# Kernel optimization log

Hardware: AMD Instinct MI355X
Metric: run time of the kernel (lower is better)

The kernel has to match this reference:

```python
import jax, jax.numpy as jnp
import numpy as np

KNB = 64  # max_num_neighbors in torch_geometric radius query


def fps(p, n):
    # Farthest point sampling, deterministic start at index 0. p: [N,3] -> [n] int32
    N = p.shape[0]
    def step(carry, _):
        d, last = carry
        d = jnp.minimum(d, jnp.sum((p - p[last]) ** 2, -1))
        return (d, jnp.argmax(d).astype(jnp.int32)), last
    _, idx = jax.lax.scan(step, (jnp.full((N,), jnp.inf, p.dtype), jnp.int32(0)), None, length=n)
    return idx


def mlp3(h, w1, b1, w2, b2, w3, b3):
    # torch_geometric-style MLP: Lin+ReLU per layer (batch_norm disabled)
    h = jax.nn.relu(h @ w1 + b1)
    h = jax.nn.relu(h @ w2 + b2)
    return jax.nn.relu(h @ w3 + b3)


def sa_module(x, pos, S, r, params):
    # PointNet++ set abstraction: FPS -> ball query -> per-edge MLP -> max pool.
    # x: [B,N,C], pos: [B,N,3] -> ([B,S,Cout], [B,S,3])
    B, N, _ = pos.shape
    idx = jax.vmap(lambda p: fps(p, S))(pos)                           # [B,S]
    ctr = jnp.take_along_axis(pos, idx[:, :, None], 1)                 # [B,S,3]
    d2 = jnp.sum((ctr[:, :, None, :] - pos[:, None, :, :]) ** 2, -1)   # [B,S,N]
    mask = d2 <= r * r
    # first KNB in-radius points in index order (emulates radius() neighbor cap)
    score = jnp.where(mask, (N - jnp.arange(N, dtype=jnp.int32))[None, None, :], 0)
    vals, nb = jax.lax.top_k(score, KNB)                               # [B,S,KNB]
    valid = vals > 0
    flat = nb.reshape(B, S * KNB)
    xj = jnp.take_along_axis(x, flat[:, :, None], 1).reshape(B, S, KNB, -1)
    pj = jnp.take_along_axis(pos, flat[:, :, None], 1).reshape(B, S, KNB, 3)
    feat = jnp.concatenate([xj, pj - ctr[:, :, None, :]], -1)          # [B,S,KNB,C+3]
    h = mlp3(feat, *params)
    h = jnp.where(valid[..., None], h, -jnp.inf)
    return h.max(axis=2), ctr                                          # max-aggr over ball


def setup_inputs() -> dict:
    key = jax.random.key(0)
    ks = jax.random.split(key, 64)
    inp = {}
    inp["x"] = jax.random.normal(ks[0], (16, 2048, 9), jnp.float32)
    inp["pos"] = jax.random.uniform(ks[1], (16, 2048, 3), dtype=jnp.float32)
    i = 2
    for tag, c0, c1, c2, c3 in [("s1", 12, 64, 64, 128), ("s2", 131, 128, 128, 256),
                                 ("s3", 259, 256, 512, 1024), ("f", 1024, 512, 512, 256)]:
        for j, (ci, co) in enumerate([(c0, c1), (c1, c2), (c2, c3)], 1):
            inp[f"{tag}w{j}"] = jax.random.normal(ks[i], (ci, co), jnp.float32) / np.sqrt(ci); i += 1
            inp[f"{tag}b{j}"] = jnp.zeros((co,), jnp.float32)
    for j, (ci, co) in enumerate([(1024, 512), (512, 256), (256, 256), (256, 128), (128, 128)], 1):
        inp[f"l{j}w"] = jax.random.normal(ks[i], (ci, co), jnp.float32) / np.sqrt(ci); i += 1
        inp[f"l{j}b"] = jnp.zeros((co,), jnp.float32)
    return inp


def reference(x, pos,
              s1w1, s1b1, s1w2, s1b2, s1w3, s1b3,
              s2w1, s2b1, s2w2, s2b2, s2w3, s2b3,
              s3w1, s3b1, s3w2, s3b2, s3w3, s3b3,
              fw1, fb1, fw2, fb2, fw3, fb3,
              l1w, l1b, l2w, l2b, l3w, l3b, l4w, l4b, l5w, l5b):
    KP1 = 4  # K+1 frames per sample; B = n_batch*(K+1)
    x1, p1 = sa_module(x, pos, 1024, 0.2, (s1w1, s1b1, s1w2, s1b2, s1w3, s1b3))
    x2, p2 = sa_module(x1, p1, 256, 0.4, (s2w1, s2b1, s2w2, s2b2, s2w3, s2b3))
    # GlobalSAModule: MLP then global max pool over remaining points
    g = mlp3(jnp.concatenate([x2, p2], -1), s3w1, s3b1, s3w2, s3b2, s3w3, s3b3).max(axis=1)  # [B,1024]
    h = jax.nn.relu(g @ l1w + l1b)
    h = jax.nn.relu(h @ l2w + l2b)
    h = h @ l3w + l3b                       # [B,256]
    h = h.reshape(-1, KP1 * 256)            # [n_batch, 1024]
    h = mlp3(h, fw1, fb1, fw2, fb2, fw3, fb3)  # fusion_type == 0
    h = jax.nn.relu(h @ l4w + l4b)
    return h @ l5w + l5b                    # [n_batch, z_dim=128]
```

## Files before the change

kernel.cpp:

```cpp
#include <hip/hip_runtime.h>
#include <cstddef>

#define DEVINF __builtin_inff()

typedef __attribute__((ext_vector_type(8))) short bf16x8;
typedef __attribute__((ext_vector_type(4))) float f32x4;
typedef __attribute__((ext_vector_type(2))) float f32x2;

__device__ __forceinline__ unsigned short f2bf(float x) {
  unsigned u = __float_as_uint(x);
  return (unsigned short)((u + 0x7fff + ((u >> 16) & 1)) >> 16);
}
__device__ __forceinline__ float bf2f(unsigned short h) {
  return __uint_as_float(((unsigned)h) << 16);
}
__device__ __forceinline__ void split_bf(float x, unsigned short& hi, unsigned short& lo) {
  hi = f2bf(x);
  lo = f2bf(x - bf2f(hi));
}

#define FPS_RED_LEVEL(CTRL)                                                      \
  {                                                                              \
    int th = __builtin_amdgcn_update_dpp((int)hi, (int)hi, CTRL, 0xf, 0xf, false); \
    int tl = __builtin_amdgcn_update_dpp((int)lo, (int)lo, CTRL, 0xf, 0xf, false); \
    bool take = ((unsigned)th > hi) || (((unsigned)th == hi) && ((unsigned)tl > lo)); \
    hi = take ? (unsigned)th : hi;                                               \
    lo = take ? (unsigned)tl : lo;                                               \
  }

template <int PPLH, int NCH>
__device__ __forceinline__ unsigned long long fps_wave_step(
    f32x2* qx, f32x2* qy, f32x2* qz, f32x2* d, float lx, float ly, float lz,
    int lane, int ibase) {
#pragma clang fp contract(off)
  const int CH = PPLH / NCH;
  float bv[NCH];
  int bi[NCH];
#pragma unroll
  for (int c = 0; c < NCH; ++c) { bv[c] = -DEVINF; bi[c] = 0x7fffffff; }
  f32x2 lxv = {lx, lx}, lyv = {ly, ly}, lzv = {lz, lz};
#pragma unroll
  for (int h = 0; h < PPLH; ++h) {
    const int c = h / CH;
    f32x2 dx = qx[h] - lxv, dy = qy[h] - lyv, dz = qz[h] - lzv;
    f32x2 t0 = dx * dx, t1 = dy * dy, t2 = dz * dz;
    f32x2 d2 = (t0 + t1) + t2;
    f32x2 dn;
    dn.x = fminf(d[h].x, d2.x);
    dn.y = fminf(d[h].y, d2.y);
    d[h] = dn;
    int i0 = ibase + (2 * h) * 64 + lane;
    if (dn.x > bv[c]) { bv[c] = dn.x; bi[c] = i0; }
    if (dn.y > bv[c]) { bv[c] = dn.y; bi[c] = i0 + 64; }
  }
  unsigned hi, lo;
  if (NCH == 4) {
    unsigned h0 = __float_as_uint(bv[0]), l0 = ~(unsigned)bi[0];
    unsigned h1 = __float_as_uint(bv[1]), l1 = ~(unsigned)bi[1];
    unsigned h2 = __float_as_uint(bv[2]), l2 = ~(unsigned)bi[2];
    unsigned h3 = __float_as_uint(bv[3]), l3 = ~(unsigned)bi[3];
    bool t01 = (h1 > h0) || ((h1 == h0) && (l1 > l0));
    unsigned ha = t01 ? h1 : h0, la = t01 ? l1 : l0;
    bool t23 = (h3 > h2) || ((h3 == h2) && (l3 > l2));
    unsigned hb = t23 ? h3 : h2, lb = t23 ? l3 : l2;
    bool tab = (hb > ha) || ((hb == ha) && (lb > la));
    hi = tab ? hb : ha;
    lo = tab ? lb : la;
  } else {
    const int c1 = (NCH > 1) ? 1 : 0;
    unsigned h0 = __float_as_uint(bv[0]), l0 = ~(unsigned)bi[0];
    unsigned h1 = __float_as_uint(bv[c1]), l1 = ~(unsigned)bi[c1];
    bool t01 = (h1 > h0) || ((h1 == h0) && (l1 > l0));
    hi = t01 ? h1 : h0;
    lo = t01 ? l1 : l0;
  }
  FPS_RED_LEVEL(0x111)
  FPS_RED_LEVEL(0x112)
  FPS_RED_LEVEL(0x114)
  FPS_RED_LEVEL(0x118)
  FPS_RED_LEVEL(0x142)
  FPS_RED_LEVEL(0x143)
  return (((unsigned long long)hi) << 32) | lo;
}

struct PrepJobs {
  const float* src[9];
  unsigned short* hi[9];
  unsigned short* lo[9];
  int K[9], N[9], rl[9];
  int blk0[10];
};

__global__ __launch_bounds__(256, 1) void fps1_prep_kernel(
    const float* __restrict__ pos, float* __restrict__ p1, PrepJobs jb) {
#pragma clang fp contract(off)
  const int tid = threadIdx.x;
  if (blockIdx.x >= 16) {
    int blk = blockIdx.x - 16;
    int j = 0;
#pragma unroll
    for (int t = 1; t < 9; ++t)
      if (blk >= jb.blk0[t]) j = t;
    int idx = (blk - jb.blk0[j]) * 256 + tid;
    int rl = jb.rl[j], N = jb.N[j], K = jb.K[j];
    if (idx >= N * rl) return;
    int n = idx / rl, k = idx - n * rl;
    float v = (k < K) ? jb.src[j][(size_t)k * N + n] : 0.f;
    unsigned short h, l;
    split_bf(v, h, l);
    jb.hi[j][idx] = h;
    jb.lo[j][idx] = l;
    return;
  }
  const int b = blockIdx.x;
  const int w = tid >> 6, lane = tid & 63;
  __shared__ __align__(16) float4 p4[2048];
  __shared__ __align__(16) float4 carr[1024];
  __shared__ unsigned long long kv[2][4];
  f32x2 qx[4], qy[4], qz[4], d[4];
  const int ibase = w * 512;
#pragma unroll
  for (int h = 0; h < 4; ++h) {
    int i0 = ibase + (2 * h) * 64 + lane, i1 = i0 + 64;
    const float* a = pos + ((size_t)b * 2048 + i0) * 3;
    const float* c = pos + ((size_t)b * 2048 + i1) * 3;
    float x0 = a[0], y0 = a[1], z0 = a[2];
    float x1 = c[0], y1 = c[1], z1 = c[2];
    qx[h].x = x0; qx[h].y = x1;
    qy[h].x = y0; qy[h].y = y1;
    qz[h].x = z0; qz[h].y = z1;
    d[h].x = DEVINF; d[h].y = DEVINF;
    p4[i0] = float4{x0, y0, z0, 0.f};
    p4[i1] = float4{x1, y1, z1, 0.f};
  }
  __syncthreads();
  int last = 0;
  for (int s = 0; s < 1024; ++s) {
    float4 c4 = p4[last];
    if (tid == 0) carr[s] = c4;
    unsigned long long k =
        fps_wave_step<4, 4>(qx, qy, qz, d, c4.x, c4.y, c4.z, lane, ibase);
    if (lane == 63) kv[s & 1][w] = k;
    __syncthreads();
    unsigned long long k0 = kv[s & 1][0], k1 = kv[s & 1][1];
    unsigned long long k2 = kv[s & 1][2], k3 = kv[s & 1][3];
    unsigned long long ka = k0 > k1 ? k0 : k1;
    unsigned long long kb = k2 > k3 ? k2 : k3;
    unsigned long long kk = ka > kb ? ka : kb;
    last = (int)~(unsigned)kk;
  }
  for (int i = tid; i < 1024; i += 256) {
    float4 c = carr[i];
    p1[((size_t)b * 1024 + i) * 3 + 0] = c.x;
    p1[((size_t)b * 1024 + i) * 3 + 1] = c.y;
    p1[((size_t)b * 1024 + i) * 3 + 2] = c.z;
  }
}

template <int KS, int T>
__device__ __forceinline__ void mfma_allm(
    const unsigned short* __restrict__ inHi, const unsigned short* __restrict__ inLo,
    int sIn, const unsigned short* __restrict__ wHi,
    const unsigned short* __restrict__ wLo, int rl, const float* __restrict__ bias,
    int n0, int lane, f32x4 acc[4][T]) {
  const int col = lane & 15, quad = lane >> 4;
#pragma unroll
  for (int t = 0; t < T; ++t) {
    float bv = bias[n0 + t * 16 + col];
#pragma unroll
    for (int mt = 0; mt < 4; ++mt) {
      acc[mt][t].x = bv; acc[mt][t].y = bv; acc[mt][t].z = bv; acc[mt][t].w = bv;
    }
  }
  size_t b0 = (size_t)(n0 + col) * rl + quad * 8;
  bf16x8 bh = *(const bf16x8*)(wHi + b0);
  bf16x8 bl = *(const bf16x8*)(wLo + b0);
#pragma unroll 1
  for (int ks = 0; ks < KS; ++ks) {
    bf16x8 ah[4], al[4];
#pragma unroll
    for (int mt = 0; mt < 4; ++mt) {
      int aoff = (mt * 16 + col) * sIn + ks * 32 + quad * 8;
      ah[mt] = *(const bf16x8*)(inHi + aoff);
      al[mt] = *(const bf16x8*)(inLo + aoff);
    }
#pragma unroll
    for (int t = 0; t < T; ++t) {
      int nks = (t + 1 < T) ? ks : ks + 1;
      int nt = (t + 1 < T) ? t + 1 : 0;
      if (nks > KS - 1) nks = KS - 1;
      size_t nboff = (size_t)(n0 + nt * 16 + col) * rl + nks * 32 + quad * 8;
      bf16x8 nh = *(const bf16x8*)(wHi + nboff);
      bf16x8 nl = *(const bf16x8*)(wLo + nboff);
#pragma unroll
      for (int mt = 0; mt < 4; ++mt) {
        acc[mt][t] = __builtin_amdgcn_mfma_f32_16x16x32_bf16(ah[mt], bh, acc[mt][t], 0, 0, 0);
        acc[mt][t] = __builtin_amdgcn_mfma_f32_16x16x32_bf16(ah[mt], bl, acc[mt][t], 0, 0, 0);
        acc[mt][t] = __builtin_amdgcn_mfma_f32_16x16x32_bf16(al[mt], bh, acc[mt][t], 0, 0, 0);
      }
      bh = nh;
      bl = nl;
    }
  }
}

template <int T>
__device__ __forceinline__ void store_allm(const f32x4 acc[4][T], int n0,
                                           unsigned short* outHi,
                                           unsigned short* outLo, int sOut,
                                           int lane) {
  const int col = lane & 15, quad = lane >> 4;
// ... 40 lines not shown
    const unsigned short* __restrict__ inHi, const unsigned short* __restrict__ inLo,
    int sIn, const unsigned short* __restrict__ wHi,
    const unsigned short* __restrict__ wLo, int rl, const float* __restrict__ bias,
    int n0, int lane, f32x4 acc[T]) {
  const int col = lane & 15, quad = lane >> 4;
#pragma unroll
  for (int t = 0; t < T; ++t) {
    float bv = bias[n0 + t * 16 + col];
    acc[t].x = bv; acc[t].y = bv; acc[t].z = bv; acc[t].w = bv;
  }
  size_t b0 = (size_t)(n0 + col) * rl + quad * 8;
  bf16x8 bh = *(const bf16x8*)(wHi + b0);
  bf16x8 bl = *(const bf16x8*)(wLo + b0);
#pragma unroll 1
  for (int ks = 0; ks < KS; ++ks) {
    int aoff = col * sIn + ks * 32 + quad * 8;
    bf16x8 ah = *(const bf16x8*)(inHi + aoff);
    bf16x8 al = *(const bf16x8*)(inLo + aoff);
#pragma unroll
    for (int t = 0; t < T; ++t) {
      int nks = (t + 1 < T) ? ks : ks + 1;
      int nt = (t + 1 < T) ? t + 1 : 0;
      if (nks > KS - 1) nks = KS - 1;
      size_t nboff = (size_t)(n0 + nt * 16 + col) * rl + nks * 32 + quad * 8;
      bf16x8 nh = *(const bf16x8*)(wHi + nboff);
      bf16x8 nl = *(const bf16x8*)(wLo + nboff);
      acc[t] = __builtin_amdgcn_mfma_f32_16x16x32_bf16(ah, bh, acc[t], 0, 0, 0);
      acc[t] = __builtin_amdgcn_mfma_f32_16x16x32_bf16(ah, bl, acc[t], 0, 0, 0);
      acc[t] = __builtin_amdgcn_mfma_f32_16x16x32_bf16(al, bh, acc[t], 0, 0, 0);
      bh = nh;
      bl = nl;
    }
  }
}

template <int T>
__device__ __forceinline__ void store_1m(const f32x4 acc[T], int n0,
                                         unsigned short* outHi,
                                         unsigned short* outLo, int sOut, int lane) {
  const int col = lane & 15, quad = lane >> 4;
#pragma unroll
  for (int t = 0; t < T; ++t)
#pragma unroll
    for (int r = 0; r < 4; ++r) {
      int p = quad * 4 + r;
      float v = fmaxf(acc[t][r], 0.f);
      unsigned short h, l;
      split_bf(v, h, l);
      outHi[p * sOut + n0 + t * 16 + col] = h;
      outLo[p * sOut + n0 + t * 16 + col] = l;
    }
}

__global__ __launch_bounds__(256, 4) void sa1_kernel(
    const float* __restrict__ x,
    const float* __restrict__ pos,
    const float* __restrict__ ctr,
    float* __restrict__ p2,
    const unsigned short* __restrict__ w1h, const unsigned short* __restrict__ w1l,
    const unsigned short* __restrict__ w2h, const unsigned short* __restrict__ w2l,
    const unsigned short* __restrict__ w3h, const unsigned short* __restrict__ w3l,
    const float* __restrict__ b1, const float* __restrict__ b2,
    const float* __restrict__ b3,
    float* __restrict__ out)
{
  const int N = 2048;
  const float r2 = (float)(0.2 * 0.2);
  const int tid = threadIdx.x;
  const int w = tid >> 6, lane = tid & 63;
  __shared__ __align__(16) unsigned short smem[4 * 4608];
  unsigned short* bufA_hi = smem;
  unsigned short* bufA_lo = smem + 4608;
  unsigned short* bufB_hi = smem + 9216;
  unsigned short* bufB_lo = smem + 13824;
  __shared__ int nb[64];
  __shared__ int tot[4];
  __shared__ unsigned long long kv2[2][4];

  if (blockIdx.x < 16) {
    const int bb = blockIdx.x;
    float4* q4 = (float4*)smem;
    float4* carr = (float4*)(smem + 8192);
    for (int i = tid; i < 1024; i += 256) {
      const float* pr = ctr + ((size_t)bb * 1024 + i) * 3;
      q4[i] = float4{pr[0], pr[1], pr[2], 0.f};
    }
    __syncthreads();
    f32x2 qx[2], qy[2], qz[2], d[2];
    const int ibase = w * 256;
#pragma unroll
    for (int h = 0; h < 2; ++h) {
      int i0 = ibase + (2 * h) * 64 + lane, i1 = i0 + 64;
      float4 a = q4[i0], c = q4[i1];
      qx[h].x = a.x; qx[h].y = c.x;
      qy[h].x = a.y; qy[h].y = c.y;
      qz[h].x = a.z; qz[h].y = c.z;
      d[h].x = DEVINF; d[h].y = DEVINF;
    }
    int last = 0;
    for (int s = 0; s < 256; ++s) {
      float4 c4 = q4[last];
      if (tid == 0) carr[s] = c4;
      unsigned long long k =
          fps_wave_step<2, 2>(qx, qy, qz, d, c4.x, c4.y, c4.z, lane, ibase);
      if (lane == 63) kv2[s & 1][w] = k;
      __syncthreads();
      unsigned long long k0 = kv2[s & 1][0], k1 = kv2[s & 1][1];
      unsigned long long k2 = kv2[s & 1][2], k3 = kv2[s & 1][3];
      unsigned long long ka = k0 > k1 ? k0 : k1;
      unsigned long long kb = k2 > k3 ? k2 : k3;
      unsigned long long kk = ka > kb ? ka : kb;
      last = (int)~(unsigned)kk;
    }
    {
      float4 c = carr[tid];
      if (tid < 256) {
        p2[((size_t)bb * 256 + tid) * 3 + 0] = c.x;
        p2[((size_t)bb * 256 + tid) * 3 + 1] = c.y;
        p2[((size_t)bb * 256 + tid) * 3 + 2] = c.z;
      }
    }
    return;
  }

  const int bs = blockIdx.x - 16;
  const int b = bs >> 10;
  const float cx = ctr[bs * 3 + 0], cy = ctr[bs * 3 + 1], cz = ctr[bs * 3 + 2];
  nb[lane] = 0;
  unsigned long long mloc[8];
  {
#pragma clang fp contract(off)
#pragma unroll
    for (int it = 0; it < 8; ++it) {
      int i = (w * 8 + it) * 64 + lane;
      const float* p = pos + ((size_t)b * N + i) * 3;
      float dx = p[0] - cx, dy = p[1] - cy, dz = p[2] - cz;
      float t0 = dx * dx, t1 = dy * dy, t2 = dz * dz;
      float d2 = (t0 + t1) + t2;
      mloc[it] = __ballot(d2 <= r2);
    }
  }
  {
    int mytot = 0;
#pragma unroll
    for (int it = 0; it < 8; ++it) mytot += (int)__popcll(mloc[it]);
    if (lane == 0) tot[w] = mytot;
  }
  __syncthreads();
  const int t0s = tot[0], t1s = tot[1], t2s = tot[2], t3s = tot[3];
  {
    int cnt = (w > 0 ? t0s : 0) + (w > 1 ? t1s : 0) + (w > 2 ? t2s : 0);
#pragma unroll
    for (int it = 0; it < 8; ++it) {
      unsigned long long m = mloc[it];
      bool inr = (m >> lane) & 1;
      int posn = cnt + (int)__popcll(m & ((1ull << lane) - 1ull));
      if (inr && posn < 64) nb[posn] = (w * 8 + it) * 64 + lane;
      cnt += (int)__popcll(m);
    }
  }
  const int total = t0s + t1s + t2s + t3s;
  const int nvalid = total < 64 ? total : 64;
  __syncthreads();
  {
    int j = nb[lane];
    if (w < 3) {
      const float* xr = x + ((size_t)b * N + j) * 9 + w * 3;
      float f0 = xr[0], f1 = xr[1], f2 = xr[2];
      unsigned short h, l;
      split_bf(f0, h, l); bufA_hi[lane * 72 + w * 3 + 0] = h; bufA_lo[lane * 72 + w * 3 + 0] = l;
      split_bf(f1, h, l); bufA_hi[lane * 72 + w * 3 + 1] = h; bufA_lo[lane * 72 + w * 3 + 1] = l;
      split_bf(f2, h, l); bufA_hi[lane * 72 + w * 3 + 2] = h; bufA_lo[lane * 72 + w * 3 + 2] = l;
    } else {
      const float* pr = pos + ((size_t)b * N + j) * 3;
      float rr[3] = {pr[0] - cx, pr[1] - cy, pr[2] - cz};
#pragma unroll
      for (int c = 0; c < 3; ++c) {
        unsigned short h, l;
        split_bf(rr[c], h, l);
        bufA_hi[lane * 72 + 9 + c] = h;
        bufA_lo[lane * 72 + 9 + c] = l;
      }
#pragma unroll
      for (int k = 12; k < 32; ++k) {
        bufA_hi[lane * 72 + k] = 0;
        bufA_lo[lane * 72 + k] = 0;
      }
    }
  }
  __syncthreads();
  {
    f32x4 acc[4][1];
    mfma_allm<1, 1>(bufA_hi, bufA_lo, 72, w1h, w1l, 40, b1, w * 16, lane, acc);
    store_allm<1>(acc, w * 16, bufB_hi, bufB_lo, 72, lane);
  }
  __syncthreads();
  {
    f32x4 acc[4][1];
    mfma_allm<2, 1>(bufB_hi, bufB_lo, 72, w2h, w2l, 72, b2, w * 16, lane, acc);
    store_allm<1>(acc, w * 16, bufA_hi, bufA_lo, 72, lane);
  }
  __syncthreads();
  {
    f32x4 acc[4][2];
    mfma_allm<2, 2>(bufA_hi, bufA_lo, 72, w3h, w3l, 72, b3, w * 32, lane, acc);
    outpool_allm<2>(acc, w * 32, out + (size_t)bs * 128, nvalid, lane);
  }
}

__global__ __launch_bounds__(256, 2) void sa2_kernel(
    const float* __restrict__ x1,
    const float* __restrict__ pos1,
    const float* __restrict__ ctr,
    const unsigned short* __restrict__ w1h, const unsigned short* __restrict__ w1l,
    const unsigned short* __restrict__ w2h, const unsigned short* __restrict__ w2l,
    const unsigned short* __restrict__ w3h, const unsigned short* __restrict__ w3l,
    const float* __restrict__ b1, const float* __restrict__ b2,
    const float* __restrict__ b3,
    float* __restrict__ out)
{
  const int N = 1024;
  const float r2 = (float)(0.4 * 0.4);
  const int bs = blockIdx.x;
  const int b = bs >> 8;
  const int tid = threadIdx.x;
  const int w = tid >> 6, lane = tid & 63;
  const float cx = ctr[bs * 3 + 0], cy = ctr[bs * 3 + 1], cz = ctr[bs * 3 + 2];
  __shared__ __align__(16) unsigned short bufA_hi[64 * 168], bufA_lo[64 * 168];
  __shared__ __align__(16) unsigned short bufB_hi[64 * 136], bufB_lo[64 * 136];
  __shared__ int nb[64];
  __shared__ int tot[4];
  nb[lane] = 0;
  unsigned long long mloc[4];
  {
#pragma clang fp contract(off)
#pragma unroll
    for (int it = 0; it < 4; ++it) {
      int i = (w * 4 + it) * 64 + lane;
      const float* p = pos1 + ((size_t)b * N + i) * 3;
      float dx = p[0] - cx, dy = p[1] - cy, dz = p[2] - cz;
      float t0 = dx * dx, t1 = dy * dy, t2 = dz * dz;
      float d2 = (t0 + t1) + t2;
      mloc[it] = __ballot(d2 <= r2);
    }
  }
  {
    int mytot = 0;
#pragma unroll
    for (int it = 0; it < 4; ++it) mytot += (int)__popcll(mloc[it]);
    if (lane == 0) tot[w] = mytot;
  }
  __syncthreads();
  const int t0s = tot[0], t1s = tot[1], t2s = tot[2], t3s = tot[3];
  {
    int cnt = (w > 0 ? t0s : 0) + (w > 1 ? t1s : 0) + (w > 2 ? t2s : 0);
#pragma unroll
    for (int it = 0; it < 4; ++it) {
      unsigned long long m = mloc[it];
      bool inr = (m >> lane) & 1;
// ... 207 lines not shown
#pragma unroll 4
    for (int k = 0; k < 1024; ++k) {
      float v = A[k];
      a0 = fmaf(v, fw1[(size_t)k * 512 + tid], a0);
      a1 = fmaf(v, fw1[(size_t)k * 512 + tid + 256], a1);
    }
    Bf[tid] = fmaxf(a0, 0.f);
    Bf[tid + 256] = fmaxf(a1, 0.f);
  }
  __syncthreads();
  {
    float a0 = fb2[tid], a1 = fb2[tid + 256];
#pragma unroll 4
    for (int k = 0; k < 512; ++k) {
      float v = Bf[k];
      a0 = fmaf(v, fw2[(size_t)k * 512 + tid], a0);
      a1 = fmaf(v, fw2[(size_t)k * 512 + tid + 256], a1);
    }
    __syncthreads();
    A[tid] = fmaxf(a0, 0.f);
    A[tid + 256] = fmaxf(a1, 0.f);
  }
  __syncthreads();
  {
    float a = fb3[tid];
#pragma unroll 4
    for (int k = 0; k < 512; ++k) a = fmaf(A[k], fw3[(size_t)k * 256 + tid], a);
    __syncthreads();
    Bf[tid] = fmaxf(a, 0.f);
  }
  __syncthreads();
  {
    if (tid < 128) {
      float a = l4b[tid];
#pragma unroll 4
      for (int k = 0; k < 256; ++k) a = fmaf(Bf[k], l4w[(size_t)k * 128 + tid], a);
      A[tid] = fmaxf(a, 0.f);
    }
  }
  __syncthreads();
  {
    if (tid < 128) {
      float a = l5b[tid];
#pragma unroll 4
      for (int k = 0; k < 128; ++k) a = fmaf(A[k], l5w[(size_t)k * 128 + tid], a);
      out[(size_t)m * 128 + tid] = a;
    }
  }
}

extern "C" void kernel_launch(void* const* d_in, const int* in_sizes, int n_in,
                              void* d_out, int out_size, void* d_ws, size_t ws_size,
                              hipStream_t stream) {
  (void)in_sizes; (void)n_in; (void)out_size; (void)ws_size;
  const float* x    = (const float*)d_in[0];
  const float* pos  = (const float*)d_in[1];
  const float* s1w1 = (const float*)d_in[2];  const float* s1b1 = (const float*)d_in[3];
  const float* s1w2 = (const float*)d_in[4];  const float* s1b2 = (const float*)d_in[5];
  const float* s1w3 = (const float*)d_in[6];  const float* s1b3 = (const float*)d_in[7];
  const float* s2w1 = (const float*)d_in[8];  const float* s2b1 = (const float*)d_in[9];
  const float* s2w2 = (const float*)d_in[10]; const float* s2b2 = (const float*)d_in[11];
  const float* s2w3 = (const float*)d_in[12]; const float* s2b3 = (const float*)d_in[13];
  const float* s3w1 = (const float*)d_in[14]; const float* s3b1 = (const float*)d_in[15];
  const float* s3w2 = (const float*)d_in[16]; const float* s3b2 = (const float*)d_in[17];
  const float* s3w3 = (const float*)d_in[18]; const float* s3b3 = (const float*)d_in[19];
  const float* fw1  = (const float*)d_in[20]; const float* fb1  = (const float*)d_in[21];
  const float* fw2  = (const float*)d_in[22]; const float* fb2  = (const float*)d_in[23];
  const float* fw3  = (const float*)d_in[24]; const float* fb3  = (const float*)d_in[25];
  const float* l1w  = (const float*)d_in[26]; const float* l1b  = (const float*)d_in[27];
  const float* l2w  = (const float*)d_in[28]; const float* l2b  = (const float*)d_in[29];
  const float* l3w  = (const float*)d_in[30]; const float* l3b  = (const float*)d_in[31];
  const float* l4w  = (const float*)d_in[32]; const float* l4b  = (const float*)d_in[33];
  const float* l5w  = (const float*)d_in[34]; const float* l5b  = (const float*)d_in[35];
  float* out = (float*)d_out;

  float* ws = (float*)d_ws;
  float* p1   = ws;
  float* x1   = p1 + 49152;
  float* p2   = x1 + 2097152;
  float* x2   = p2 + 12288;
  float* part = x2 + 1048576;
  float* hC   = part + 262144;
  unsigned short* wp = (unsigned short*)(hC + 4096);
  unsigned short* s1w1h = wp;              unsigned short* s1w1l = s1w1h + 2560;
  unsigned short* s1w2h = s1w1l + 2560;    unsigned short* s1w2l = s1w2h + 4608;
  unsigned short* s1w3h = s1w2l + 4608;    unsigned short* s1w3l = s1w3h + 9216;
  unsigned short* s2w1h = s1w3l + 9216;    unsigned short* s2w1l = s2w1h + 21504;
  unsigned short* s2w2h = s2w1l + 21504;   unsigned short* s2w2l = s2w2h + 17408;
  unsigned short* s2w3h = s2w2l + 17408;   unsigned short* s2w3l = s2w3h + 34816;
  unsigned short* g1h   = s2w3l + 34816;   unsigned short* g1l   = g1h + 75776;
  unsigned short* g2h   = g1l + 75776;     unsigned short* g2l   = g2h + 135168;
  unsigned short* g3h   = g2l + 135168;    unsigned short* g3l   = g3h + 532480;

  PrepJobs jb;
  const float* srcs[9] = {s1w1, s1w2, s1w3, s2w1, s2w2, s2w3, s3w1, s3w2, s3w3};
  unsigned short* his[9] = {s1w1h, s1w2h, s1w3h, s2w1h, s2w2h, s2w3h, g1h, g2h, g3h};
  unsigned short* los[9] = {s1w1l, s1w2l, s1w3l, s2w1l, s2w2l, s2w3l, g1l, g2l, g3l};
  int Ks[9]  = {12, 64, 64, 131, 128, 128, 259, 256, 512};
  int Ns[9]  = {64, 64, 128, 128, 128, 256, 256, 512, 1024};
  int rls[9] = {40, 72, 72, 168, 136, 136, 296, 264, 520};
  int acc_blk = 0;
  for (int j = 0; j < 9; ++j) {
    jb.src[j] = srcs[j]; jb.hi[j] = his[j]; jb.lo[j] = los[j];
    jb.K[j] = Ks[j]; jb.N[j] = Ns[j]; jb.rl[j] = rls[j];
    jb.blk0[j] = acc_blk;
    acc_blk += (Ns[j] * rls[j] + 255) / 256;
  }
  jb.blk0[9] = acc_blk;

  fps1_prep_kernel<<<16 + acc_blk, 256, 0, stream>>>(pos, p1, jb);
  sa1_kernel<<<16 * 1024 + 16, 256, 0, stream>>>(x, pos, p1, p2, s1w1h, s1w1l,
                                                 s1w2h, s1w2l, s1w3h, s1w3l,
                                                 s1b1, s1b2, s1b3, x1);
  sa2_kernel<<<16 * 256, 256, 0, stream>>>(x1, p1, p2, s2w1h, s2w1l, s2w2h,
                                           s2w2l, s2w3h, s2w3l, s2b1, s2b2,
                                           s2b3, x2);
  gsa_kernel<<<256, 256, 0, stream>>>(x2, p2, g1h, g1l, g2h, g2l, g3h, g3l,
                                      s3b1, s3b2, s3b3, part);
  head1_kernel<<<16, 256, 0, stream>>>(part, l1w, l1b, l2w, l2b, l3w, l3b, hC);
  head2_kernel<<<4, 256, 0, stream>>>(hC, fw1, fb1, fw2, fb2, fw3, fb3, l4w,
                                      l4b, l5w, l5b, out);
}
```

Before: 1.401 ms.

## Run farthest point sampling in a single wavefront to remove block barriers

Both FPS loops (stage 1 over 2048 points, stage 2 over 1024) now run on one 64-lane wave per batch instead of four waves joined by __syncthreads and a shared-memory argmax exchange each step. Each lane holds more points in registers (16 or 8 pairs), and the winning index is taken with a DPP reduction plus readlane. Centers are written straight to global memory by lane 0 rather than buffered in shared memory. This removes a block barrier per step but puts four times the distance work on each lane, which lengthens the serial chain and raises register use.

```diff
diff --git a/kernel.cpp b/kernel.cpp
--- a/kernel.cpp
+++ b/kernel.cpp
@@ -28,16 +28,17 @@
     lo = take ? (unsigned)tl : lo;                                               \
   }
 
-template <int PPLH, int NCH>
-__device__ __forceinline__ unsigned long long fps_wave_step(
-    f32x2* qx, f32x2* qy, f32x2* qz, f32x2* d, float lx, float ly, float lz,
-    int lane, int ibase) {
+template <int PPLH>
+__device__ __forceinline__ int fps_solo_step(
+    f32x2* qx, f32x2* qy, f32x2* qz, f32x2* d,
+    float lx, float ly, float lz, int lane) {
 #pragma clang fp contract(off)
+  const int NCH = 4;
   const int CH = PPLH / NCH;
   float bv[NCH];
-  int bi[NCH];
-#pragma unroll
-  for (int c = 0; c < NCH; ++c) { bv[c] = -DEVINF; bi[c] = 0x7fffffff; }
+  int bh[NCH];
+#pragma unroll
+  for (int c = 0; c < NCH; ++c) { bv[c] = -DEVINF; bh[c] = 0; }
   f32x2 lxv = {lx, lx}, lyv = {ly, ly}, lzv = {lz, lz};
 #pragma unroll
   for (int h = 0; h < PPLH; ++h) {
@@ -49,38 +50,28 @@
     dn.x = fminf(d[h].x, d2.x);
     dn.y = fminf(d[h].y, d2.y);
     d[h] = dn;
-    int i0 = ibase + (2 * h) * 64 + lane;
-    if (dn.x > bv[c]) { bv[c] = dn.x; bi[c] = i0; }
-    if (dn.y > bv[c]) { bv[c] = dn.y; bi[c] = i0 + 64; }
-  }
-  unsigned hi, lo;
-  if (NCH == 4) {
-    unsigned h0 = __float_as_uint(bv[0]), l0 = ~(unsigned)bi[0];
-    unsigned h1 = __float_as_uint(bv[1]), l1 = ~(unsigned)bi[1];
-    unsigned h2 = __float_as_uint(bv[2]), l2 = ~(unsigned)bi[2];
-    unsigned h3 = __float_as_uint(bv[3]), l3 = ~(unsigned)bi[3];
-    bool t01 = (h1 > h0) || ((h1 == h0) && (l1 > l0));
-    unsigned ha = t01 ? h1 : h0, la = t01 ? l1 : l0;
-    bool t23 = (h3 > h2) || ((h3 == h2) && (l3 > l2));
-    unsigned hb = t23 ? h3 : h2, lb = t23 ? l3 : l2;
-    bool tab = (hb > ha) || ((hb == ha) && (lb > la));
-    hi = tab ? hb : ha;
-    lo = tab ? lb : la;
-  } else {
-    const int c1 = (NCH > 1) ? 1 : 0;
-    unsigned h0 = __float_as_uint(bv[0]), l0 = ~(unsigned)bi[0];
-    unsigned h1 = __float_as_uint(bv[c1]), l1 = ~(unsigned)bi[c1];
-    bool t01 = (h1 > h0) || ((h1 == h0) && (l1 > l0));
-    hi = t01 ? h1 : h0;
-    lo = t01 ? l1 : l0;
-  }
+    if (dn.x > bv[c]) { bv[c] = dn.x; bh[c] = h * 128; }
+    if (dn.y > bv[c]) { bv[c] = dn.y; bh[c] = h * 128 + 64; }
+  }
+  unsigned h0 = __float_as_uint(bv[0]), l0 = ~(unsigned)(bh[0] + lane);
+  unsigned h1 = __float_as_uint(bv[1]), l1 = ~(unsigned)(bh[1] + lane);
+  unsigned h2 = __float_as_uint(bv[2]), l2 = ~(unsigned)(bh[2] + lane);
+  unsigned h3 = __float_as_uint(bv[3]), l3 = ~(unsigned)(bh[3] + lane);
+  bool t01 = (h1 > h0) || ((h1 == h0) && (l1 > l0));
+  unsigned ha = t01 ? h1 : h0, la = t01 ? l1 : l0;
+  bool t23 = (h3 > h2) || ((h3 == h2) && (l3 > l2));
+  unsigned hb = t23 ? h3 : h2, lb = t23 ? l3 : l2;
+  bool tab = (hb > ha) || ((hb == ha) && (lb > la));
+  unsigned hi = tab ? hb : ha;
+  unsigned lo = tab ? lb : la;
   FPS_RED_LEVEL(0x111)
   FPS_RED_LEVEL(0x112)
   FPS_RED_LEVEL(0x114)
   FPS_RED_LEVEL(0x118)
   FPS_RED_LEVEL(0x142)
   FPS_RED_LEVEL(0x143)
-  return (((unsigned long long)hi) << 32) | lo;
+  unsigned wl = (unsigned)__builtin_amdgcn_readlane((int)lo, 63);
+  return (int)~wl;
 }
 
 struct PrepJobs {
@@ -113,15 +104,13 @@
     return;
   }
   const int b = blockIdx.x;
-  const int w = tid >> 6, lane = tid & 63;
+  if (tid >= 64) return;
+  const int lane = tid;
   __shared__ __align__(16) float4 p4[2048];
-  __shared__ __align__(16) float4 carr[1024];
-  __shared__ unsigned long long kv[2][4];
-  f32x2 qx[4], qy[4], qz[4], d[4];
-  const int ibase = w * 512;
-#pragma unroll
-  for (int h = 0; h < 4; ++h) {
-    int i0 = ibase + (2 * h) * 64 + lane, i1 = i0 + 64;
+  f32x2 qx[16], qy[16], qz[16], d[16];
+#pragma unroll
+  for (int h = 0; h < 16; ++h) {
+    int i0 = h * 128 + lane, i1 = i0 + 64;
     const float* a = pos + ((size_t)b * 2048 + i0) * 3;
     const float* c = pos + ((size_t)b * 2048 + i1) * 3;
     float x0 = a[0], y0 = a[1], z0 = a[2];
@@ -133,27 +122,20 @@
     p4[i0] = float4{x0, y0, z0, 0.f};
     p4[i1] = float4{x1, y1, z1, 0.f};
   }
-  __syncthreads();
-  int last = 0;
+  float cx = __uint_as_float((unsigned)__builtin_amdgcn_readlane((int)__float_as_uint(qx[0].x), 0));
+  float cy = __uint_as_float((unsigned)__builtin_amdgcn_readlane((int)__float_as_uint(qy[0].x), 0));
+  float cz = __uint_as_float((unsigned)__builtin_amdgcn_readlane((int)__float_as_uint(qz[0].x), 0));
+  float* p1b = p1 + (size_t)b * 1024 * 3;
   for (int s = 0; s < 1024; ++s) {
+    if (lane == 0) {
+      p1b[3 * s + 0] = cx;
+      p1b[3 * s + 1] = cy;
+      p1b[3 * s + 2] = cz;
+    }
+    if (s == 1023) break;
+    int last = fps_solo_step<16>(qx, qy, qz, d, cx, cy, cz, lane);
     float4 c4 = p4[last];
-    if (tid == 0) carr[s] = c4;
-    unsigned long long k =
-        fps_wave_step<4, 4>(qx, qy, qz, d, c4.x, c4.y, c4.z, lane, ibase);
-    if (lane == 63) kv[s & 1][w] = k;
-    __syncthreads();
-    unsigned long long k0 = kv[s & 1][0], k1 = kv[s & 1][1];
-    unsigned long long k2 = kv[s & 1][2], k3 = kv[s & 1][3];
-    unsigned long long ka = k0 > k1 ? k0 : k1;
-    unsigned long long kb = k2 > k3 ? k2 : k3;
-    unsigned long long kk = ka > kb ? ka : kb;
-    last = (int)~(unsigned)kk;
-  }
-  for (int i = tid; i < 1024; i += 256) {
-    float4 c = carr[i];
-    p1[((size_t)b * 1024 + i) * 3 + 0] = c.x;
-    p1[((size_t)b * 1024 + i) * 3 + 1] = c.y;
-    p1[((size_t)b * 1024 + i) * 3 + 2] = c.z;
+    cx = c4.x; cy = c4.y; cz = c4.z;
   }
 }
 
@@ -326,50 +308,40 @@
   unsigned short* bufB_lo = smem + 13824;
   __shared__ int nb[64];
   __shared__ int tot[4];
-  __shared__ unsigned long long kv2[2][4];
 
   if (blockIdx.x < 16) {
     const int bb = blockIdx.x;
+    if (tid >= 64) return;
     float4* q4 = (float4*)smem;
-    float4* carr = (float4*)(smem + 8192);
-    for (int i = tid; i < 1024; i += 256) {
-      const float* pr = ctr + ((size_t)bb * 1024 + i) * 3;
-      q4[i] = float4{pr[0], pr[1], pr[2], 0.f};
-    }
-    __syncthreads();
-    f32x2 qx[2], qy[2], qz[2], d[2];
-    const int ibase = w * 256;
-#pragma unroll
-    for (int h = 0; h < 2; ++h) {
-      int i0 = ibase + (2 * h) * 64 + lane, i1 = i0 + 64;
-      float4 a = q4[i0], c = q4[i1];
-      qx[h].x = a.x; qx[h].y = c.x;
-      qy[h].x = a.y; qy[h].y = c.y;
-      qz[h].x = a.z; qz[h].y = c.z;
+    f32x2 qx[8], qy[8], qz[8], d[8];
+#pragma unroll
+    for (int h = 0; h < 8; ++h) {
+      int i0 = h * 128 + lane, i1 = i0 + 64;
+      const float* a = ctr + ((size_t)bb * 1024 + i0) * 3;
+      const float* c = ctr + ((size_t)bb * 1024 + i1) * 3;
+      float x0 = a[0], y0 = a[1], z0 = a[2];
+      float x1 = c[0], y1 = c[1], z1 = c[2];
+      qx[h].x = x0; qx[h].y = x1;
+      qy[h].x = y0; qy[h].y = y1;
+      qz[h].x = z0; qz[h].y = z1;
       d[h].x = DEVINF; d[h].y = DEVINF;
-    }
-    int last = 0;
+      q4[i0] = float4{x0, y0, z0, 0.f};
+      q4[i1] = float4{x1, y1, z1, 0.f};
+    }
+    float cx = __uint_as_float((unsigned)__builtin_amdgcn_readlane((int)__float_as_uint(qx[0].x), 0));
+    float cy = __uint_as_float((unsigned)__builtin_amdgcn_readlane((int)__float_as_uint(qy[0].x), 0));
+    float cz = __uint_as_float((unsigned)__builtin_amdgcn_readlane((int)__float_as_uint(qz[0].x), 0));
+    float* p2b = p2 + (size_t)bb * 256 * 3;
     for (int s = 0; s < 256; ++s) {
+      if (lane == 0) {
+        p2b[3 * s + 0] = cx;
+        p2b[3 * s + 1] = cy;
+        p2b[3 * s + 2] = cz;
+      }
+      if (s == 255) break;
+      int last = fps_solo_step<8>(qx, qy, qz, d, cx, cy, cz, lane);
       float4 c4 = q4[last];
-      if (tid == 0) carr[s] = c4;
-      unsigned long long k =
-          fps_wave_step<2, 2>(qx, qy, qz, d, c4.x, c4.y, c4.z, lane, ibase);
-      if (lane == 63) kv2[s & 1][w] = k;
-      __syncthreads();
-      unsigned long long k0 = kv2[s & 1][0], k1 = kv2[s & 1][1];
-      unsigned long long k2 = kv2[s & 1][2], k3 = kv2[s & 1][3];
-      unsigned long long ka = k0 > k1 ? k0 : k1;
-      unsigned long long kb = k2 > k3 ? k2 : k3;
-      unsigned long long kk = ka > kb ? ka : kb;
-      last = (int)~(unsigned)kk;
-    }
-    {
-      float4 c = carr[tid];
-      if (tid < 256) {
-        p2[((size_t)bb * 256 + tid) * 3 + 0] = c.x;
-        p2[((size_t)bb * 256 + tid) * 3 + 1] = c.y;
-        p2[((size_t)bb * 256 + tid) * 3 + 2] = c.z;
-      }
+      cx = c4.x; cy = c4.y; cz = c4.z;
     }
     return;
   }
```

New measurement: 1.665 ms. +18.8%, slower.

## Fuse FPS1, FPS2, weight prep and SA1 into persistent cooperative kernel

Applied to the files above, without the earlier changes.

Replaces the separate FPS1/prep launch and the SA1 launch with one persistent cooperative kernel. Sixteen blocks run FPS1 and publish each chosen centroid plus a progress counter, sixteen more wait and then run FPS2, and the rest do weight prep and then pull SA1 work items from an atomic counter, spinning until their centroid is ready. The aim is to overlap the serial FPS with the ball-query/MLP work instead of waiting for the whole FPS to finish. It adds spin-wait and atomic overhead, depends on cooperative launch and workspace size (with a fallback path), and relies on relaxed atomics plus an explicit waitcnt for memory ordering.

```diff
diff --git a/kernel.cpp b/kernel.cpp
--- a/kernel.cpp
+++ b/kernel.cpp
@@ -91,32 +91,35 @@
   int blk0[10];
 };
 
-__global__ __launch_bounds__(256, 1) void fps1_prep_kernel(
-    const float* __restrict__ pos, float* __restrict__ p1, PrepJobs jb) {
+__device__ __forceinline__ void do_prep_chunk(const PrepJobs& jb, int blk, int tid) {
+  int j = 0;
+#pragma unroll
+  for (int t = 1; t < 9; ++t)
+    if (blk >= jb.blk0[t]) j = t;
+  int idx = (blk - jb.blk0[j]) * 256 + tid;
+  int rl = jb.rl[j], N = jb.N[j], K = jb.K[j];
+  if (idx >= N * rl) return;
+  int n = idx / rl, k = idx - n * rl;
+  float v = (k < K) ? jb.src[j][(size_t)k * N + n] : 0.f;
+  unsigned short h, l;
+  split_bf(v, h, l);
+  jb.hi[j][idx] = h;
+  jb.lo[j][idx] = l;
+}
+
+__global__ __launch_bounds__(256) void prep_kernel(PrepJobs jb) {
+  do_prep_chunk(jb, (int)blockIdx.x, (int)threadIdx.x);
+}
+
+__global__ __launch_bounds__(256, 1) void fps1_kernel(
+    const float* __restrict__ pos, float* __restrict__ p1) {
 #pragma clang fp contract(off)
   const int tid = threadIdx.x;
-  if (blockIdx.x >= 16) {
-    int blk = blockIdx.x - 16;
-    int j = 0;
-#pragma unroll
-    for (int t = 1; t < 9; ++t)
-      if (blk >= jb.blk0[t]) j = t;
-    int idx = (blk - jb.blk0[j]) * 256 + tid;
-    int rl = jb.rl[j], N = jb.N[j], K = jb.K[j];
-    if (idx >= N * rl) return;
-    int n = idx / rl, k = idx - n * rl;
-    float v = (k < K) ? jb.src[j][(size_t)k * N + n] : 0.f;
-    unsigned short h, l;
-    split_bf(v, h, l);
-    jb.hi[j][idx] = h;
-    jb.lo[j][idx] = l;
-    return;
-  }
   const int b = blockIdx.x;
   const int w = tid >> 6, lane = tid & 63;
   __shared__ __align__(16) float4 p4[2048];
   __shared__ __align__(16) float4 carr[1024];
-  __shared__ unsigned long long kv[2][4];
+  __shared__ __align__(16) unsigned long long kv[2][4];
   f32x2 qx[4], qy[4], qz[4], d[4];
   const int ibase = w * 512;
 #pragma unroll
@@ -157,6 +160,47 @@
   }
 }
 
+__device__ __forceinline__ void fps2_core(float4* q4, float4* carr,
+                                          unsigned long long (*kv2)[4],
+                                          float* __restrict__ p2b, int tid,
+                                          int w, int lane) {
+#pragma clang fp contract(off)
+  f32x2 qx[2], qy[2], qz[2], d[2];
+  const int ibase = w * 256;
+#pragma unroll
+  for (int h = 0; h < 2; ++h) {
+    int i0 = ibase + (2 * h) * 64 + lane, i1 = i0 + 64;
+    float4 a = q4[i0], c = q4[i1];
+    qx[h].x = a.x; qx[h].y = c.x;
+    qy[h].x = a.y; qy[h].y = c.y;
+    qz[h].x = a.z; qz[h].y = c.z;
+    d[h].x = DEVINF; d[h].y = DEVINF;
+  }
+  int last = 0;
+  for (int s = 0; s < 256; ++s) {
+    float4 c4 = q4[last];
+    if (tid == 0) carr[s] = c4;
+    unsigned long long k =
+        fps_wave_step<2, 2>(qx, qy, qz, d, c4.x, c4.y, c4.z, lane, ibase);
+    if (lane == 63) kv2[s & 1][w] = k;
+    __syncthreads();
+    unsigned long long k0 = kv2[s & 1][0], k1 = kv2[s & 1][1];
+    unsigned long long k2 = kv2[s & 1][2], k3 = kv2[s & 1][3];
+    unsigned long long ka = k0 > k1 ? k0 : k1;
+    unsigned long long kb = k2 > k3 ? k2 : k3;
+    unsigned long long kk = ka > kb ? ka : kb;
+    last = (int)~(unsigned)kk;
+  }
+  {
+    float4 c = carr[tid];
+    if (tid < 256) {
+      p2b[3 * tid + 0] = c.x;
+      p2b[3 * tid + 1] = c.y;
+      p2b[3 * tid + 2] = c.z;
+    }
+  }
+}
+
 template <int KS, int T>
 __device__ __forceinline__ void mfma_allm(
     const unsigned short* __restrict__ inHi, const unsigned short* __restrict__ inLo,
@@ -303,80 +347,20 @@
     }
 }
 
-__global__ __launch_bounds__(256, 4) void sa1_kernel(
-    const float* __restrict__ x,
-    const float* __restrict__ pos,
-    const float* __restrict__ ctr,
-    float* __restrict__ p2,
+__device__ __forceinline__ void sa1_body(
+    int b, int bs, float cx, float cy, float cz,
+    const float* __restrict__ x, const float* __restrict__ pos,
     const unsigned short* __restrict__ w1h, const unsigned short* __restrict__ w1l,
     const unsigned short* __restrict__ w2h, const unsigned short* __restrict__ w2l,
     const unsigned short* __restrict__ w3h, const unsigned short* __restrict__ w3l,
     const float* __restrict__ b1, const float* __restrict__ b2,
-    const float* __restrict__ b3,
-    float* __restrict__ out)
-{
+    const float* __restrict__ b3, float* __restrict__ out,
+    unsigned short* bufA_hi, unsigned short* bufA_lo,
+    unsigned short* bufB_hi, unsigned short* bufB_lo, int* nb, int* tot) {
   const int N = 2048;
   const float r2 = (float)(0.2 * 0.2);
   const int tid = threadIdx.x;
   const int w = tid >> 6, lane = tid & 63;
-  __shared__ __align__(16) unsigned short smem[4 * 4608];
-  unsigned short* bufA_hi = smem;
-  unsigned short* bufA_lo = smem + 4608;
-  unsigned short* bufB_hi = smem + 9216;
-  unsigned short* bufB_lo = smem + 13824;
-  __shared__ int nb[64];
-  __shared__ int tot[4];
-  __shared__ unsigned long long kv2[2][4];
-
-  if (blockIdx.x < 16) {
-    const int bb = blockIdx.x;
-    float4* q4 = (float4*)smem;
-    float4* carr = (float4*)(smem + 8192);
-    for (int i = tid; i < 1024; i += 256) {
-      const float* pr = ctr + ((size_t)bb * 1024 + i) * 3;
-      q4[i] = float4{pr[0], pr[1], pr[2], 0.f};
-    }
-    __syncthreads();
-    f32x2 qx[2], qy[2], qz[2], d[2];
-    const int ibase = w * 256;
-#pragma unroll
-    for (int h = 0; h < 2; ++h) {
-      int i0 = ibase + (2 * h) * 64 + lane, i1 = i0 + 64;
-      float4 a = q4[i0], c = q4[i1];
-      qx[h].x = a.x; qx[h].y = c.x;
-      qy[h].x = a.y; qy[h].y = c.y;
-      qz[h].x = a.z; qz[h].y = c.z;
-      d[h].x = DEVINF; d[h].y = DEVINF;
-    }
-    int last = 0;
-    for (int s = 0; s < 256; ++s) {
-      float4 c4 = q4[last];
-      if (tid == 0) carr[s] = c4;
-      unsigned long long k =
-          fps_wave_step<2, 2>(qx, qy, qz, d, c4.x, c4.y, c4.z, lane, ibase);
-      if (lane == 63) kv2[s & 1][w] = k;
-      __syncthreads();
-      unsigned long long k0 = kv2[s & 1][0], k1 = kv2[s & 1][1];
-      unsigned long long k2 = kv2[s & 1][2], k3 = kv2[s & 1][3];
-      unsigned long long ka = k0 > k1 ? k0 : k1;
-      unsigned long long kb = k2 > k3 ? k2 : k3;
-      unsigned long long kk = ka > kb ? ka : kb;
-      last = (int)~(unsigned)kk;
-    }
-    {
-      float4 c = carr[tid];
-      if (tid < 256) {
-        p2[((size_t)bb * 256 + tid) * 3 + 0] = c.x;
-        p2[((size_t)bb * 256 + tid) * 3 + 1] = c.y;
-        p2[((size_t)bb * 256 + tid) * 3 + 2] = c.z;
-      }
-    }
-    return;
-  }
-
-  const int bs = blockIdx.x - 16;
-  const int b = bs >> 10;
-  const float cx = ctr[bs * 3 + 0], cy = ctr[bs * 3 + 1], cz = ctr[bs * 3 + 2];
   nb[lane] = 0;
   unsigned long long mloc[8];
   {
@@ -456,6 +440,163 @@
     f32x4 acc[4][2];
     mfma_allm<2, 2>(bufA_hi, bufA_lo, 72, w3h, w3l, 72, b3, w * 32, lane, acc);
     outpool_allm<2>(acc, w * 32, out + (size_t)bs * 128, nvalid, lane);
+  }
+}
+
+__global__ __launch_bounds__(256, 4) void sa1_kernel(
+    const float* __restrict__ x, const float* __restrict__ pos,
+    const float* __restrict__ ctr, float* __restrict__ p2,
+    const unsigned short* __restrict__ w1h, const unsigned short* __restrict__ w1l,
+    const unsigned short* __restrict__ w2h, const unsigned short* __restrict__ w2l,
+    const unsigned short* __restrict__ w3h, const unsigned short* __restrict__ w3l,
+    const float* __restrict__ b1, const float* __restrict__ b2,
+    const float* __restrict__ b3, float* __restrict__ out) {
+  const int tid = threadIdx.x;
+  const int w = tid >> 6, lane = tid & 63;
+  __shared__ __align__(16) unsigned short smem[4 * 4608];
+  __shared__ int nb[64];
+  __shared__ int tot[4];
+  __shared__ __align__(16) unsigned long long kv2s[2][4];
+  if (blockIdx.x < 16) {
+    const int bb = blockIdx.x;
+    float4* q4 = (float4*)smem;
+    float4* carr = (float4*)(smem + 8192);
+    for (int i = tid; i < 1024; i += 256) {
+      const float* pr = ctr + ((size_t)bb * 1024 + i) * 3;
+      q4[i] = float4{pr[0], pr[1], pr[2], 0.f};
+    }
+    __syncthreads();
+    fps2_core(q4, carr, kv2s, p2 + (size_t)bb * 768, tid, w, lane);
+    return;
+  }
+  const int bs = blockIdx.x - 16;
+  const int b = bs >> 10;
+  const float cx = ctr[bs * 3 + 0], cy = ctr[bs * 3 + 1], cz = ctr[bs * 3 + 2];
+  sa1_body(b, bs, cx, cy, cz, x, pos, w1h, w1l, w2h, w2l, w3h, w3l, b1, b2, b3,
+           out, smem, smem + 4608, smem + 9216, smem + 13824, nb, tot);
+}
+
+struct FusedParams {
+  const float* x; const float* pos; float* p1; float* p2;
+  const unsigned short *w1h, *w1l, *w2h, *w2l, *w3h, *w3l;
+  const float *b1, *b2, *b3;
+  float* x1;
+  int* prog; int* wctr;
+  PrepJobs jb;
+  int nprep;
+  int ncons;
+};
+
+__global__ __launch_bounds__(256, 4) void fused_kernel(FusedParams P) {
+  const int tid = threadIdx.x;
+  const int w = tid >> 6, lane = tid & 63;
+  __shared__ __align__(16) char lds[37184];
+  if (blockIdx.x < 16) {
+#pragma clang fp contract(off)
+    __builtin_amdgcn_s_setprio(3);
+    const int b = blockIdx.x;
+    float4* p4 = (float4*)lds;
+    unsigned long long(*kv)[4] = (unsigned long long(*)[4])(lds + 32768);
+    f32x2 qx[4], qy[4], qz[4], d[4];
+    const int ibase = w * 512;
+#pragma unroll
+    for (int h = 0; h < 4; ++h) {
+      int i0 = ibase + (2 * h) * 64 + lane, i1 = i0 + 64;
+      const float* a = P.pos + ((size_t)b * 2048 + i0) * 3;
+      const float* c = P.pos + ((size_t)b * 2048 + i1) * 3;
+      float x0 = a[0], y0 = a[1], z0 = a[2];
+      float x1 = c[0], y1 = c[1], z1 = c[2];
+      qx[h].x = x0; qx[h].y = x1;
+      qy[h].x = y0; qy[h].y = y1;
+      qz[h].x = z0; qz[h].y = z1;
+      d[h].x = DEVINF; d[h].y = DEVINF;
+      p4[i0] = float4{x0, y0, z0, 0.f};
+      p4[i1] = float4{x1, y1, z1, 0.f};
+    }
+    __syncthreads();
+    unsigned* p1u = (unsigned*)P.p1 + (size_t)b * 3072;
+    int last = 0;
+    for (int s = 0; s < 1024; ++s) {
+      float4 c4 = p4[last];
+      if (tid == 0) {
+        if (s > 0) {
+          asm volatile("s_waitcnt vmcnt(0)" ::: "memory");
+          __hip_atomic_store(P.prog + b, s, __ATOMIC_RELAXED, __HIP_MEMORY_SCOPE_AGENT);
+        }
+        __hip_atomic_store(p1u + 3 * s + 0, __float_as_uint(c4.x), __ATOMIC_RELAXED, __HIP_MEMORY_SCOPE_AGENT);
+        __hip_atomic_store(p1u + 3 * s + 1, __float_as_uint(c4.y), __ATOMIC_RELAXED, __HIP_MEMORY_SCOPE_AGENT);
+        __hip_atomic_store(p1u + 3 * s + 2, __float_as_uint(c4.z), __ATOMIC_RELAXED, __HIP_MEMORY_SCOPE_AGENT);
+      }
+      unsigned long long k =
+          fps_wave_step<4, 4>(qx, qy, qz, d, c4.x, c4.y, c4.z, lane, ibase);
+      if (lane == 63) kv[s & 1][w] = k;
+      __syncthreads();
+      unsigned long long k0 = kv[s & 1][0], k1 = kv[s & 1][1];
+      unsigned long long k2 = kv[s & 1][2], k3 = kv[s & 1][3];
+      unsigned long long ka = k0 > k1 ? k0 : k1;
+      unsigned long long kb = k2 > k3 ? k2 : k3;
+      unsigned long long kk = ka > kb ? ka : kb;
+      last = (int)~(unsigned)kk;
+    }
+    if (tid == 0) {
+      asm volatile("s_waitcnt vmcnt(0)" ::: "memory");
+      __hip_atomic_store(P.prog + b, 1024, __ATOMIC_RELAXED, __HIP_MEMORY_SCOPE_AGENT);
+    }
+    return;
+  }
+  if (blockIdx.x < 32) {
+    const int bb = blockIdx.x - 16;
+    float4* q4 = (float4*)lds;
+    float4* carr = (float4*)(lds + 16384);
+    unsigned long long(*kv2)[4] = (unsigned long long(*)[4])(lds + 20480);
+    if (tid == 0) {
+      while (__hip_atomic_load(P.prog + bb, __ATOMIC_RELAXED, __HIP_MEMORY_SCOPE_AGENT) < 1024)
+        __builtin_amdgcn_s_sleep(64);
+    }
+    __syncthreads();
+    __builtin_amdgcn_s_setprio(1);
+    const unsigned* p1u = (const unsigned*)P.p1 + (size_t)bb * 3072;
+    for (int i = tid; i < 1024; i += 256) {
+      float xx = __uint_as_float(__hip_atomic_load(p1u + 3 * i + 0, __ATOMIC_RELAXED, __HIP_MEMORY_SCOPE_AGENT));
+      float yy = __uint_as_float(__hip_atomic_load(p1u + 3 * i + 1, __ATOMIC_RELAXED, __HIP_MEMORY_SCOPE_AGENT));
+      float zz = __uint_as_float(__hip_atomic_load(p1u + 3 * i + 2, __ATOMIC_RELAXED, __HIP_MEMORY_SCOPE_AGENT));
+      q4[i] = float4{xx, yy, zz, 0.f};
+    }
+    __syncthreads();
+    fps2_core(q4, carr, kv2, P.p2 + (size_t)bb * 768, tid, w, lane);
+    return;
+  }
+  const int cid = blockIdx.x - 32;
+  for (int blk = cid; blk < P.nprep; blk += P.ncons)
+    do_prep_chunk(P.jb, blk, tid);
+  unsigned short* bufA_hi = (unsigned short*)lds;
+  unsigned short* bufA_lo = (unsigned short*)(lds + 9216);
+  unsigned short* bufB_hi = (unsigned short*)(lds + 18432);
+  unsigned short* bufB_lo = (unsigned short*)(lds + 27648);
+  int* nb = (int*)(lds + 36864);
+  int* tot = (int*)(lds + 37120);
+  int* sh_w = (int*)(lds + 37136);
+  float* shc = (float*)(lds + 37140);
+  const unsigned* p1u = (const unsigned*)P.p1;
+  for (;;) {
+    if (tid == 0) sh_w[0] = atomicAdd(P.wctr, 1);
+    __syncthreads();
+    int iw = sh_w[0];
+    if (iw >= 16384) break;
+    int s = iw >> 4, b = iw & 15;
+    if (tid == 0) {
+      while (__hip_atomic_load(P.prog + b, __ATOMIC_RELAXED, __HIP_MEMORY_SCOPE_AGENT) <= s)
+        __builtin_amdgcn_s_sleep(64);
+      const unsigned* cp = p1u + (size_t)b * 3072 + 3 * s;
+      shc[0] = __uint_as_float(__hip_atomic_load(cp + 0, __ATOMIC_RELAXED, __HIP_MEMORY_SCOPE_AGENT));
+      shc[1] = __uint_as_float(__hip_atomic_load(cp + 1, __ATOMIC_RELAXED, __HIP_MEMORY_SCOPE_AGENT));
+      shc[2] = __uint_as_float(__hip_atomic_load(cp + 2, __ATOMIC_RELAXED, __HIP_MEMORY_SCOPE_AGENT));
+    }
+    __syncthreads();
+    sa1_body(b, b * 1024 + s, shc[0], shc[1], shc[2], P.x, P.pos, P.w1h, P.w1l,
+             P.w2h, P.w2l, P.w3h, P.w3l, P.b1, P.b2, P.b3, P.x1, bufA_hi,
+             bufA_lo, bufB_hi, bufB_lo, nb, tot);
+    __syncthreads();
   }
 }
 
@@ -769,7 +910,7 @@
 extern "C" void kernel_launch(void* const* d_in, const int* in_sizes, int n_in,
                               void* d_out, int out_size, void* d_ws, size_t ws_size,
                               hipStream_t stream) {
-  (void)in_sizes; (void)n_in; (void)out_size; (void)ws_size;
+  (void)in_sizes; (void)n_in; (void)out_size;
   const float* x    = (const float*)d_in[0];
   const float* pos  = (const float*)d_in[1];
   const float* s1w1 = (const float*)d_in[2];  const float* s1b1 = (const float*)d_in[3];
@@ -808,27 +949,86 @@
   unsigned short* g1h   = s2w3l + 34816;   unsigned short* g1l   = g1h + 75776;
   unsigned short* g2h   = g1l + 75776;     unsigned short* g2l   = g2h + 135168;
   unsigned short* g3h   = g2l + 135168;    unsigned short* g3l   = g3h + 532480;
-
-  PrepJobs jb;
-  const float* srcs[9] = {s1w1, s1w2, s1w3, s2w1, s2w2, s2w3, s3w1, s3w2, s3w3};
-  unsigned short* his[9] = {s1w1h, s1w2h, s1w3h, s2w1h, s2w2h, s2w3h, g1h, g2h, g3h};
-  unsigned short* los[9] = {s1w1l, s1w2l, s1w3l, s2w1l, s2w2l, s2w3l, g1l, g2l, g3l};
-  int Ks[9]  = {12, 64, 64, 131, 128, 128, 259, 256, 512};
-  int Ns[9]  = {64, 64, 128, 128, 128, 256, 256, 512, 1024};
-  int rls[9] = {40, 72, 72, 168, 136, 136, 296, 264, 520};
-  int acc_blk = 0;
-  for (int j = 0; j < 9; ++j) {
-    jb.src[j] = srcs[j]; jb.hi[j] = his[j]; jb.lo[j] = los[j];
-    jb.K[j] = Ks[j]; jb.N[j] = Ns[j]; jb.rl[j] = rls[j];
-    jb.blk0[j] = acc_blk;
-    acc_blk += (Ns[j] * rls[j] + 255) / 256;
-  }
-  jb.blk0[9] = acc_blk;
-
-  fps1_prep_kernel<<<16 + acc_blk, 256, 0, stream>>>(pos, p1, jb);
-  sa1_kernel<<<16 * 1024 + 16, 256, 0, stream>>>(x, pos, p1, p2, s1w1h, s1w1l,
-                                                 s1w2h, s1w2l, s1w3h, s1w3l,
-                                                 s1b1, s1b2, s1b3, x1);
+  int* ctrl = (int*)(g3l + 532480);
+  int* prog = ctrl;
+  int* wctr = ctrl + 16;
+
+  PrepJobs jbA{};
+  {
+    const float* s[3] = {s1w1, s1w2, s1w3};
+    unsigned short* hs[3] = {s1w1h, s1w2h, s1w3h};
+    unsigned short* ls[3] = {s1w1l, s1w2l, s1w3l};
+    int Ks[3] = {12, 64, 64}, Ns[3] = {64, 64, 128}, rls[3] = {40, 72, 72};
+    int acc = 0;
+    for (int j = 0; j < 3; ++j) {
+      jbA.src[j] = s[j]; jbA.hi[j] = hs[j]; jbA.lo[j] = ls[j];
+      jbA.K[j] = Ks[j]; jbA.N[j] = Ns[j]; jbA.rl[j] = rls[j];
+      jbA.blk0[j] = acc;
+      acc += (Ns[j] * rls[j] + 255) / 256;
+    }
+    for (int j = 3; j < 9; ++j) jbA.blk0[j] = 0x7fffffff;
+    jbA.blk0[9] = acc;
+  }
+  PrepJobs jbB{};
+  int accB = 0;
+  {
+    const float* s[6] = {s2w1, s2w2, s2w3, s3w1, s3w2, s3w3};
+    unsigned short* hs[6] = {s2w1h, s2w2h, s2w3h, g1h, g2h, g3h};
+    unsigned short* ls[6] = {s2w1l, s2w2l, s2w3l, g1l, g2l, g3l};
+    int Ks[6] = {131, 128, 128, 259, 256, 512};
+    int Ns[6] = {128, 128, 256, 256, 512, 1024};
+    int rls[6] = {168, 136, 136, 296, 264, 520};
+    for (int j = 0; j < 6; ++j) {
+      jbB.src[j] = s[j]; jbB.hi[j] = hs[j]; jbB.lo[j] = ls[j];
+      jbB.K[j] = Ks[j]; jbB.N[j] = Ns[j]; jbB.rl[j] = rls[j];
+      jbB.blk0[j] = accB;
+      accB += (Ns[j] * rls[j] + 255) / 256;
+    }
+    for (int j = 6; j < 9; ++j) jbB.blk0[j] = 0x7fffffff;
+    jbB.blk0[9] = accB;
+  }
+
+  bool try_coop = (ws_size >= 17227844ull);
+  static int gblocks = -2;
+  if (try_coop) {
+    if (gblocks == -2) {
+      int dev = 0;
+      (void)hipGetDevice(&dev);
+      int ncu = 0;
+      (void)hipDeviceGetAttribute(&ncu, hipDeviceAttributeMultiprocessorCount, dev);
+      int maxb = 0;
+      (void)hipOccupancyMaxActiveBlocksPerMultiprocessor(&maxb, (const void*)fused_kernel, 256, 0);
+      gblocks = (ncu > 0 && maxb > 0) ? ncu * maxb : -1;
+    }
+    if (gblocks < 64) try_coop = false;
+  }
+  bool coop_done = false;
+  bool prepA_done = false;
+  if (try_coop) {
+    hipMemsetAsync(ctrl, 0, 68, stream);
+    prep_kernel<<<64, 256, 0, stream>>>(jbA);
+    prepA_done = true;
+    FusedParams fp;
+    fp.x = x; fp.pos = pos; fp.p1 = p1; fp.p2 = p2;
+    fp.w1h = s1w1h; fp.w1l = s1w1l; fp.w2h = s1w2h; fp.w2l = s1w2l;
+    fp.w3h = s1w3h; fp.w3l = s1w3l;
+    fp.b1 = s1b1; fp.b2 = s1b2; fp.b3 = s1b3;
+    fp.x1 = x1; fp.prog = prog; fp.wctr = wctr;
+    fp.jb = jbB; fp.nprep = accB; fp.ncons = gblocks - 32;
+    void* kargs[] = {(void*)&fp};
+    hipError_t e = hipLaunchCooperativeKernel((const void*)fused_kernel,
+                                              dim3((unsigned)gblocks), dim3(256),
+                                              kargs, 0, stream);
+    coop_done = (e == hipSuccess);
+  }
+  if (!coop_done) {
+    if (!prepA_done) prep_kernel<<<64, 256, 0, stream>>>(jbA);
+    prep_kernel<<<accB, 256, 0, stream>>>(jbB);
+    fps1_kernel<<<16, 256, 0, stream>>>(pos, p1);
+    sa1_kernel<<<16 * 1024 + 16, 256, 0, stream>>>(x, pos, p1, p2, s1w1h, s1w1l,
+                                                   s1w2h, s1w2l, s1w3h, s1w3l,
+                                                   s1b1, s1b2, s1b3, x1);
+  }
   sa2_kernel<<<16 * 256, 256, 0, stream>>>(x1, p1, p2, s2w1h, s2w1l, s2w2h,
                                            s2w2l, s2w3h, s2w3l, s2b1, s2b2,
                                            s2b3, x2);
```

New measurement: 3.318 ms. 2.37x slower.
